# Kernel tuning notes

Hardware: AMD Instinct MI355X
Metric: run time of the kernel (lower is better)

The kernel has to match this reference:

```python
import jax, jax.numpy as jnp
import numpy as np

N, E, IN, HID, HEADS, OUT = 50000, 800000, 128, 32, 4, 2
NEG = 0.2   # LeakyReLU negative slope (PyG default)
EPS = 1e-5  # BatchNorm eps


def setup_inputs() -> dict:
    key = jax.random.key(0)
    ks = jax.random.split(key, 32)
    g = lambda i, shape, s=0.05: (jax.random.normal(ks[i], shape, jnp.float32) * s)
    d = {
        'x': jax.random.normal(ks[0], (N, IN), jnp.float32),
        'edge_index': jax.random.randint(ks[1], (2, E), 0, N, jnp.int32),
        'edge_attr': jax.random.normal(ks[2], (E, 1), jnp.float32),
        # conv1: GATv2, in=IN, out=HID, heads=HEADS, edge_dim=1
        'c1_Wl': g(3, (IN, HEADS * HID)), 'c1_bl': g(4, (HEADS * HID,)),
        'c1_Wr': g(5, (IN, HEADS * HID)), 'c1_br': g(6, (HEADS * HID,)),
        'c1_We': g(7, (1, HEADS * HID)),
        'c1_att': g(8, (HEADS, HID)),
        'c1_bias': g(9, (HEADS * HID,)),
        'bn1_gamma': jnp.ones((HEADS * HID,), jnp.float32),
        'bn1_beta': jnp.zeros((HEADS * HID,), jnp.float32),
        'bn1_mean': g(10, (HEADS * HID,)),
        'bn1_var': jax.random.uniform(ks[11], (HEADS * HID,), jnp.float32, 0.5, 1.5),
        # conv2: GATv2, in=HEADS*HID, out=HID, heads=1, edge_dim=1
        'c2_Wl': g(12, (HEADS * HID, HID)), 'c2_bl': g(13, (HID,)),
        'c2_Wr': g(14, (HEADS * HID, HID)), 'c2_br': g(15, (HID,)),
        'c2_We': g(16, (1, HID)),
        'c2_att': g(17, (1, HID)),
        'c2_bias': g(18, (HID,)),
        'bn2_gamma': jnp.ones((HID,), jnp.float32),
        'bn2_beta': jnp.zeros((HID,), jnp.float32),
        'bn2_mean': g(19, (HID,)),
        'bn2_var': jax.random.uniform(ks[20], (HID,), jnp.float32, 0.5, 1.5),
        # classifier
        'clf_W': g(21, (HID, OUT)), 'clf_b': g(22, (OUT,)),
    }
    return d


def _gatv2(x, src, dst, eattr, Wl, bl, Wr, br, We, att, bias, heads, out_ch, concat):
    n = x.shape[0]
    xl = (x @ Wl + bl).reshape(n, heads, out_ch)   # source transform
    xr = (x @ Wr + br).reshape(n, heads, out_ch)   # target transform
    el = (eattr @ We).reshape(-1, heads, out_ch)   # edge transform (no bias in PyG)
    s = xl[src] + xr[dst] + el                     # [E, H, C]
    s = jnp.where(s > 0, s, NEG * s)               # LeakyReLU
    logits = jnp.einsum('ehc,hc->eh', s, att)      # [E, H]
    # segment softmax over destination nodes (every node has a self-loop)
    m = jax.ops.segment_max(logits, dst, num_segments=n)
    a = jnp.exp(logits - m[dst])
    denom = jax.ops.segment_sum(a, dst, num_segments=n)
    alpha = a / denom[dst]                         # [E, H]
    out = jax.ops.segment_sum(alpha[:, :, None] * xl[src], dst, num_segments=n)
    out = out.reshape(n, heads * out_ch) if concat else out.mean(axis=1)
    return out + bias


def _bn_eval(x, gamma, beta, mean, var):
    return (x - mean) * (gamma / jnp.sqrt(var + EPS)) + beta


def reference(x, edge_index, edge_attr,
              c1_Wl, c1_bl, c1_Wr, c1_br, c1_We, c1_att, c1_bias,
              bn1_gamma, bn1_beta, bn1_mean, bn1_var,
              c2_Wl, c2_bl, c2_Wr, c2_br, c2_We, c2_att, c2_bias,
              bn2_gamma, bn2_beta, bn2_mean, bn2_var,
              clf_W, clf_b):
    n = x.shape[0]
    # add self-loops once (PyG GATv2 default add_self_loops=True, fill_value='mean')
    loop = jnp.arange(n, dtype=edge_index.dtype)
    src = jnp.concatenate([edge_index[0], loop])
    dst = jnp.concatenate([edge_index[1], loop])
    loop_attr = jnp.broadcast_to(edge_attr.mean(axis=0, keepdims=True), (n, edge_attr.shape[1]))
    eattr = jnp.concatenate([edge_attr, loop_attr], axis=0)

    h = _gatv2(x, src, dst, eattr, c1_Wl, c1_bl, c1_Wr, c1_br, c1_We, c1_att, c1_bias,
               HEADS, HID, True)
    h = jax.nn.relu(_bn_eval(h, bn1_gamma, bn1_beta, bn1_mean, bn1_var))
    # dropout inactive in eval mode
    h = _gatv2(h, src, dst, eattr, c2_Wl, c2_bl, c2_Wr, c2_br, c2_We, c2_att, c2_bias,
               1, HID, True)
    h = jax.nn.relu(_bn_eval(h, bn2_gamma, bn2_beta, bn2_mean, bn2_var))
    return h @ clf_W + clf_b
```

## Files before the change

### kernel.cpp

```cpp
#include <hip/hip_runtime.h>

#define NNODES 50000
#define NEDGES 800000
#define ETOT   850000
#define IN_CH  128
#define HID    32
#define HEADS  4
#define C1     128
#define NEG    0.2f
#define BNEPS  1e-5f
#define XFB2   1563
#define EHB    3125
#define WTS    160
#define XSS    136
#define NC     16
#define SCB    196

typedef __attribute__((ext_vector_type(8))) short short8;
typedef __attribute__((ext_vector_type(4))) float f32x4;

__device__ __forceinline__ unsigned short bf16r(float f) {
    unsigned u = __float_as_uint(f);
    return (unsigned short)((u + 0x7fffu + ((u >> 16) & 1u)) >> 16);
}
__device__ __forceinline__ unsigned bf16pair(float f0, float f1) {
    return (unsigned)bf16r(f0) | ((unsigned)bf16r(f1) << 16);
}
__device__ __forceinline__ float blo(unsigned u) { return __uint_as_float(u << 16); }
__device__ __forceinline__ float bhi(unsigned u) { return __uint_as_float(u & 0xffff0000u); }

__device__ __forceinline__ int block_iscan(int v, int* ls) {
    int lane = threadIdx.x & 63, w = threadIdx.x >> 6;
    #pragma unroll
    for (int o = 1; o < 64; o <<= 1) {
        int t = __shfl_up(v, o);
        if (lane >= o) v += t;
    }
    if (lane == 63) ls[w] = v;
    __syncthreads();
    int add = 0;
    #pragma unroll
    for (int i = 0; i < 4; i++) add += (i < w) ? ls[i] : 0;
    return v + add;
}

__global__ __launch_bounds__(256) void k_prep(const float* __restrict__ Wl,
                                              const float* __restrict__ Wr,
                                              unsigned short* __restrict__ WT) {
    int idx = blockIdx.x * 256 + threadIdx.x;
    int mat = idx >> 14, rem = idx & 16383;
    int k = rem >> 7, n = rem & 127;
    float v = mat ? Wr[k * 128 + n] : Wl[k * 128 + n];
    WT[(size_t)(mat * 128 + n) * WTS + k] = bf16r(v);
}

__global__ __launch_bounds__(256) void k_xf_eh(
    const float* __restrict__ x,
    const float* __restrict__ bl, const float* __restrict__ br,
    const unsigned short* __restrict__ WT,
    unsigned* __restrict__ xlb, float* __restrict__ xr,
    const int* __restrict__ ei, const float* __restrict__ ea,
    int* __restrict__ hist, float* __restrict__ meanbuf) {
    __shared__ short xs_s[64 * XSS];
    if (blockIdx.x >= XFB2) {
        float* ls = (float*)xs_s;
        int eb = blockIdx.x - XFB2;
        int e = eb * 256 + threadIdx.x;
        int c = eb & (NC - 1);
        float v = 0.f;
        if (e < NEDGES) {
            atomicAdd(&hist[c * NNODES + ei[NEDGES + e]], 1);
            v = ea[e];
        }
        #pragma unroll
        for (int o = 32; o > 0; o >>= 1) v += __shfl_down(v, o, 64);
        if ((threadIdx.x & 63) == 0) ls[threadIdx.x >> 6] = v;
        __syncthreads();
        if (threadIdx.x == 0) atomicAdd(meanbuf, ls[0] + ls[1] + ls[2] + ls[3]);
        return;
    }
    int n0g = blockIdx.x * 32;
    {
        int nd = threadIdx.x >> 3, kc = (threadIdx.x & 7) * 16;
        bool valid = (n0g + nd) < NNODES;
        float xv[16];
        #pragma unroll
        for (int i = 0; i < 4; i++) {
            float4 t = valid ? ((const float4*)(x + (size_t)(n0g + nd) * IN_CH + kc))[i]
                             : make_float4(0.f, 0.f, 0.f, 0.f);
            xv[4 * i] = t.x; xv[4 * i + 1] = t.y; xv[4 * i + 2] = t.z; xv[4 * i + 3] = t.w;
        }
        unsigned hi[8], lo[8];
        #pragma unroll
        for (int i = 0; i < 8; i++) {
            unsigned short h0 = bf16r(xv[2 * i]), h1 = bf16r(xv[2 * i + 1]);
            float l0 = xv[2 * i]     - __uint_as_float(((unsigned)h0) << 16);
            float l1 = xv[2 * i + 1] - __uint_as_float(((unsigned)h1) << 16);
            hi[i] = (unsigned)h0 | ((unsigned)h1 << 16);
            lo[i] = bf16pair(l0, l1);
        }
        uint4* ph = (uint4*)&xs_s[nd * XSS + kc];
        ph[0] = make_uint4(hi[0], hi[1], hi[2], hi[3]);
        ph[1] = make_uint4(hi[4], hi[5], hi[6], hi[7]);
        uint4* pl = (uint4*)&xs_s[(nd + 32) * XSS + kc];
        pl[0] = make_uint4(lo[0], lo[1], lo[2], lo[3]);
        pl[1] = make_uint4(lo[4], lo[5], lo[6], lo[7]);
    }
    __syncthreads();
    int lane = threadIdx.x & 63;
    int lm = lane & 15, q = lane >> 4;
    int w = threadIdx.x >> 6;
    int n0 = w * 64;
    f32x4 acc[2][4];
    #pragma unroll
    for (int mt = 0; mt < 2; mt++)
        #pragma unroll
        for (int nt = 0; nt < 4; nt++) acc[mt][nt] = (f32x4)0.f;

    #pragma unroll
    for (int ks = 0; ks < 4; ks++) {
        int k0 = ks * 32 + q * 8;
        short8 ah0 = *(const short8*)&xs_s[(lm)      * XSS + k0];
        short8 ah1 = *(const short8*)&xs_s[(16 + lm) * XSS + k0];
        short8 al0 = *(const short8*)&xs_s[(32 + lm) * XSS + k0];
        short8 al1 = *(const short8*)&xs_s[(48 + lm) * XSS + k0];
        #pragma unroll
        for (int nt = 0; nt < 4; nt++) {
            short8 bfr = *(const short8*)(WT + (size_t)(n0 + nt * 16 + lm) * WTS + k0);
            acc[0][nt] = __builtin_amdgcn_mfma_f32_16x16x32_bf16(al0, bfr, acc[0][nt], 0, 0, 0);
            acc[0][nt] = __builtin_amdgcn_mfma_f32_16x16x32_bf16(ah0, bfr, acc[0][nt], 0, 0, 0);
            acc[1][nt] = __builtin_amdgcn_mfma_f32_16x16x32_bf16(al1, bfr, acc[1][nt], 0, 0, 0);
            acc[1][nt] = __builtin_amdgcn_mfma_f32_16x16x32_bf16(ah1, bfr, acc[1][nt], 0, 0, 0);
        }
    }
    if (w < 2) {
        #pragma unroll
        for (int nt = 0; nt < 4; nt++) {
            int ch = n0 + nt * 16 + lm;
            float bv = bl[ch];
            #pragma unroll
            for (int mt = 0; mt < 2; mt++)
                #pragma unroll
                for (int r = 0; r < 4; r++) {
                    int node = n0g + mt * 16 + q * 4 + r;
                    float val = acc[mt][nt][r] + bv;
                    float pv = __shfl_xor(val, 1);
                    if ((lm & 1) == 0 && node < NNODES)
                        xlb[(size_t)node * 64 + (ch >> 1)] = bf16pair(val, pv);
                }
        }
    } else {
        #pragma unroll
        for (int nt = 0; nt < 4; nt++) {
            int ch = n0 - 128 + nt * 16 + lm;
            float bv = br[ch];
            #pragma unroll
            for (int mt = 0; mt < 2; mt++)
                #pragma unroll
                for (int r = 0; r < 4; r++) {
                    int node = n0g + mt * 16 + q * 4 + r;
                    if (node < NNODES)
                        xr[(size_t)node * C1 + ch] = acc[mt][nt][r] + bv;
                }
        }
    }
}

__global__ __launch_bounds__(256) void k_red(int* __restrict__ hist,
                                             int* __restrict__ deg,
                                             int* __restrict__ bsum) {
    __shared__ int ls[4];
    int d = blockIdx.x * 256 + threadIdx.x;
    int s = 0;
    if (d < NNODES) {
        #pragma unroll
        for (int c = 0; c < NC; c++) {
            int v = hist[c * NNODES + d];
            hist[c * NNODES + d] = s;
            s += v;
        }
        deg[d] = s;
    }
    int v = (d < NNODES) ? s + 1 : 0;
    #pragma unroll
    for (int o = 32; o > 0; o >>= 1) v += __shfl_down(v, o, 64);
    if ((threadIdx.x & 63) == 0) ls[threadIdx.x >> 6] = v;
    __syncthreads();
    if (threadIdx.x == 0) bsum[blockIdx.x] = ls[0] + ls[1] + ls[2] + ls[3];
}

__global__ __launch_bounds__(256) void k_bscan(const int* __restrict__ bsum,
                                               int* __restrict__ boff) {
    __shared__ int ls[4];
    int t = threadIdx.x;
    int v = (t < SCB) ? bsum[t] : 0;
    int incl = block_iscan(v, ls);
    if (t < SCB) boff[t] = incl - v;
}

__global__ __launch_bounds__(256) void k_rowp(const int* __restrict__ deg,
                                              const int* __restrict__ boff,
                                              int* __restrict__ rowptr) {
    __shared__ int ls[4];
    int d = blockIdx.x * 256 + threadIdx.x;
    int v = (d < NNODES) ? deg[d] + 1 : 0;
    int incl = block_iscan(v, ls);
    int base = boff[blockIdx.x];
    if (d < NNODES) rowptr[d] = base + incl - v;
    if (d == NNODES - 1) rowptr[NNODES] = base + incl;
}

__global__ __launch_bounds__(256) void k_fill(const int* __restrict__ ei,
                                              const float* __restrict__ ea,
                                              const int* __restrict__ rowptr,
                                              const float* __restrict__ meanbuf,
                                              int* __restrict__ hist,
                                              int2* __restrict__ cpack) {
    int e = blockIdx.x * 256 + threadIdx.x;
    if (e < NEDGES) {
        int d = ei[NEDGES + e];
        int c = (e >> 8) & (NC - 1);
        int off = atomicAdd(&hist[c * NNODES + d], 1);
        cpack[rowptr[d] + 1 + off] = make_int2(ei[e], __float_as_int(ea[e]));
    } else if (e < NEDGES + NNODES) {
        int i = e - NEDGES;
        cpack[rowptr[i]] = make_int2(i, __float_as_int(meanbuf[0] * (1.0f / NEDGES)));
    } else if (e < NEDGES + NNODES + 64) {
        cpack[ETOT + e - NEDGES - NNODES] = make_int2(0, 0);
    }
}

__global__ __launch_bounds__(256) void k_edge1(
    const unsigned* __restrict__ xlb, const float* __restrict__ xr,
    const int* __restrict__ rowptr, const int2* __restrict__ cpack,
    const float* __restrict__ We, const float* __restrict__ att,
    float* __restrict__ out1) {
    int node = blockIdx.x * 4 + (threadIdx.x >> 6);
    if (node >= NNODES) return;
    int lane = threadIdx.x & 63;
    int q = lane & 31, h = lane >> 5;
    int r0 = rowptr[node], r1 = rowptr[node + 1];
    float4 xrv = ((const float4*)xr)[(size_t)node * 32 + q];
    float4 wev = ((const float4*)We)[q];
    float4 atv = ((const float4*)att)[q];
    const uint2* xlv = (const uint2*)xlb;

    float den = 0.f, a0 = 0.f, a1 = 0.f, a2 = 0.f, a3 = 0.f;
    int nit = (r1 - r0 + 1) >> 1;
    int k = r0 + h;
    int2 sc = cpack[k];
    uint2 xv = xlv[(size_t)sc.x * 32 + q];
    for (int it = 0; it < nit; it++) {
        int2 scn = cpack[k + 2];
        uint2 xvn = xlv[(size_t)scn.x * 32 + q];
        bool ok = k < r1;
        float a = __int_as_float(sc.y);
        float x0 = blo(xv.x), x1 = bhi(xv.x), x2 = blo(xv.y), x3 = bhi(xv.y);
        float v0 = x0 + xrv.x + a * wev.x;  v0 = v0 > 0.f ? v0 : NEG * v0;
        float v1 = x1 + xrv.y + a * wev.y;  v1 = v1 > 0.f ? v1 : NEG * v1;
        float v2 = x2 + xrv.z + a * wev.z;  v2 = v2 > 0.f ? v2 : NEG * v2;
        float v3 = x3 + xrv.w + a * wev.w;  v3 = v3 > 0.f ? v3 : NEG * v3;
        float t = v0 * atv.x + v1 * atv.y + v2 * atv.z + v3 * atv.w;
        #pragma unroll
        for (int o = 4; o > 0; o >>= 1) t += __shfl_xor(t, o);
        float e = ok ? __expf(t) : 0.f;
        den += e;
        a0 = fmaf(e, x0, a0); a1 = fmaf(e, x1, a1);
        a2 = fmaf(e, x2, a2); a3 = fmaf(e, x3, a3);
        k += 2; sc = scn; xv = xvn;
    }
    den += __shfl_xor(den, 32);
    a0 += __shfl_xor(a0, 32); a1 += __shfl_xor(a1, 32);
    a2 += __shfl_xor(a2, 32); a3 += __shfl_xor(a3, 32);
    if (h == 0) {
        float rd = 1.f / den;
        ((float4*)out1)[(size_t)node * 32 + q] =
            make_float4(a0 * rd, a1 * rd, a2 * rd, a3 * rd);
    }
}

__global__ __launch_bounds__(256) void k_epi1(
    const float* __restrict__ out1, const float* __restrict__ bias1,
    const float* __restrict__ g1, const float* __restrict__ b1,
    const float* __restrict__ m1, const float* __restrict__ v1,
    const float* __restrict__ Wl2, const float* __restrict__ bl2,
    const float* __restrict__ Wr2, const float* __restrict__ br2,
    unsigned* __restrict__ xlb2, float* __restrict__ xr2) {
    __shared__ float hs[8 * 128];
    __shared__ float A[128], B[128];
    __shared__ float xs2[8 * 32];
    int n0 = blockIdx.x * 8;
    if (threadIdx.x < 128) {
        int c = threadIdx.x;
        float sc = g1[c] * rsqrtf(v1[c] + BNEPS);
        A[c] = sc;
        B[c] = (bias1[c] - m1[c]) * sc + b1[c];
    }
    __syncthreads();
    {
        float4 v = ((const float4*)(out1 + (size_t)n0 * C1))[threadIdx.x];
        int cb = (threadIdx.x * 4) & 127;
        float4 h;
        h.x = fmaxf(v.x * A[cb]     + B[cb],     0.f);
        h.y = fmaxf(v.y * A[cb + 1] + B[cb + 1], 0.f);
        h.z = fmaxf(v.z * A[cb + 2] + B[cb + 2], 0.f);
        h.w = fmaxf(v.w * A[cb + 3] + B[cb + 3], 0.f);
        ((float4*)hs)[threadIdx.x] = h;
    }
    __syncthreads();
    for (int o = threadIdx.x; o < 512; o += 256) {
        int node = o >> 6, rem = o & 63, mat = rem >> 5, c = rem & 31;
        const float* W = mat ? Wr2 : Wl2;
        float acc = mat ? br2[c] : bl2[c];
        const float4* hh = (const float4*)(hs + node * 128);
        #pragma unroll 8
        for (int k4 = 0; k4 < 32; k4++) {
            float4 hv = hh[k4];
            int kb = k4 * 4;
            acc += hv.x * W[kb * 32 + c]       + hv.y * W[(kb + 1) * 32 + c]
                 + hv.z * W[(kb + 2) * 32 + c] + hv.w * W[(kb + 3) * 32 + c];
        }
        if (mat) xr2[(size_t)(n0 + node) * HID + c] = acc;
        else     xs2[node * 32 + c] = acc;
    }
    __syncthreads();
    if (threadIdx.x < 128) {
        int nd = threadIdx.x >> 4, cc = threadIdx.x & 15;
        xlb2[(size_t)(n0 + nd) * 16 + cc] =
            bf16pair(xs2[nd * 32 + 2 * cc], xs2[nd * 32 + 2 * cc + 1]);
    }
}

__global__ __launch_bounds__(256) void k_edge2(
    const unsigned* __restrict__ xlb2, const float* __restrict__ xr2,
    const int* __restrict__ rowptr, const int2* __restrict__ cpack,
    const float* __restrict__ We2, const float* __restrict__ att2,
    const float* __restrict__ bias2,
    const float* __restrict__ g2, const float* __restrict__ b2,
    const float* __restrict__ m2, const float* __restrict__ v2,
    const float* __restrict__ W, const float* __restrict__ b,
    float* __restrict__ y) {
    int node = blockIdx.x * 4 + (threadIdx.x >> 6);
    if (node >= NNODES) return;
    int lane = threadIdx.x & 63;
    int q = lane & 7, s = lane >> 3;
    int r0 = rowptr[node], r1 = rowptr[node + 1];
    float4 xrv = ((const float4*)xr2)[(size_t)node * 8 + q];
    float4 wev = ((const float4*)We2)[q];
    float4 atv = ((const float4*)att2)[q];
    const uint2* xlv = (const uint2*)xlb2;

    float den = 0.f, a0 = 0.f, a1 = 0.f, a2 = 0.f, a3 = 0.f;
    int nit = (r1 - r0 + 7) >> 3;
    int k = r0 + s;
    int2 sc = cpack[k];
    uint2 xv = xlv[(size_t)sc.x * 8 + q];
    for (int it = 0; it < nit; it++) {
        int2 scn = cpack[k + 8];
        uint2 xvn = xlv[(size_t)scn.x * 8 + q];
        bool ok = k < r1;
        float a = __int_as_float(sc.y);
        float x0 = blo(xv.x), x1 = bhi(xv.x), x2 = blo(xv.y), x3 = bhi(xv.y);
        float v0 = x0 + xrv.x + a * wev.x;  v0 = v0 > 0.f ? v0 : NEG * v0;
        float v1 = x1 + xrv.y + a * wev.y;  v1 = v1 > 0.f ? v1 : NEG * v1;
        float v2 = x2 + xrv.z + a * wev.z;  v2 = v2 > 0.f ? v2 : NEG * v2;
        float v3 = x3 + xrv.w + a * wev.w;  v3 = v3 > 0.f ? v3 : NEG * v3;
        float t = v0 * atv.x + v1 * atv.y + v2 * atv.z + v3 * atv.w;
        #pragma unroll
        for (int o = 4; o > 0; o >>= 1) t += __shfl_xor(t, o);
        float e = ok ? __expf(t) : 0.f;
        den += e;
        a0 = fmaf(e, x0, a0); a1 = fmaf(e, x1, a1);
        a2 = fmaf(e, x2, a2); a3 = fmaf(e, x3, a3);
        k += 8; sc = scn; xv = xvn;
    }
    #pragma unroll
    for (int o = 8; o <= 32; o <<= 1) {
        den += __shfl_xor(den, o);
        a0 += __shfl_xor(a0, o); a1 += __shfl_xor(a1, o);
        a2 += __shfl_xor(a2, o); a3 += __shfl_xor(a3, o);
    }
    float rd = 1.f / den;
    float4 gv = ((const float4*)g2)[q],  bv = ((const float4*)b2)[q];
    float4 mv = ((const float4*)m2)[q],  vv = ((const float4*)v2)[q];
    float4 biv = ((const float4*)bias2)[q];
    float h0 = (a0 * rd + biv.x - mv.x) * (gv.x * rsqrtf(vv.x + BNEPS)) + bv.x;
    float h1 = (a1 * rd + biv.y - mv.y) * (gv.y * rsqrtf(vv.y + BNEPS)) + bv.y;
    float h2 = (a2 * rd + biv.z - mv.z) * (gv.z * rsqrtf(vv.z + BNEPS)) + bv.z;
    float h3 = (a3 * rd + biv.w - mv.w) * (gv.w * rsqrtf(vv.w + BNEPS)) + bv.w;
    h0 = fmaxf(h0, 0.f); h1 = fmaxf(h1, 0.f); h2 = fmaxf(h2, 0.f); h3 = fmaxf(h3, 0.f);
    float4 wa = ((const float4*)W)[2 * q];
    float4 wb = ((const float4*)W)[2 * q + 1];
    float t0 = h0 * wa.x + h1 * wa.z + h2 * wb.x + h3 * wb.z;
    float t1 = h0 * wa.y + h1 * wa.w + h2 * wb.y + h3 * wb.w;
    #pragma unroll
    for (int o = 4; o > 0; o >>= 1) {
        t0 += __shfl_xor(t0, o);
        t1 += __shfl_xor(t1, o);
    }
    if (lane == 0) {
        y[(size_t)node * 2]     = t0 + b[0];
        y[(size_t)node * 2 + 1] = t1 + b[1];
    }
}

extern "C" void kernel_launch(void* const* d_in, const int* in_sizes, int n_in,
                              void* d_out, int out_size, void* d_ws, size_t ws_size,
                              hipStream_t stream) {
    const float* x       = (const float*)d_in[0];
    const int*   ei      = (const int*)d_in[1];
    const float* ea      = (const float*)d_in[2];
    const float* c1_Wl   = (const float*)d_in[3];
    const float* c1_bl   = (const float*)d_in[4];
    const float* c1_Wr   = (const float*)d_in[5];
    const float* c1_br   = (const float*)d_in[6];
    const float* c1_We   = (const float*)d_in[7];
    const float* c1_att  = (const float*)d_in[8];
    const float* c1_bias = (const float*)d_in[9];
    const float* bn1_g   = (const float*)d_in[10];
    const float* bn1_b   = (const float*)d_in[11];
    const float* bn1_m   = (const float*)d_in[12];
    const float* bn1_v   = (const float*)d_in[13];
    const float* c2_Wl   = (const float*)d_in[14];
    const float* c2_bl   = (const float*)d_in[15];
    const float* c2_Wr   = (const float*)d_in[16];
    const float* c2_br   = (const float*)d_in[17];
    const float* c2_We   = (const float*)d_in[18];
    const float* c2_att  = (const float*)d_in[19];
    const float* c2_bias = (const float*)d_in[20];
    const float* bn2_g   = (const float*)d_in[21];
    const float* bn2_b   = (const float*)d_in[22];
    const float* bn2_m   = (const float*)d_in[23];
    const float* bn2_v   = (const float*)d_in[24];
    const float* clf_W   = (const float*)d_in[25];
    const float* clf_b   = (const float*)d_in[26];

    float* ws = (float*)d_ws;
    size_t off = 0;
    unsigned* XLb  = (unsigned*)(ws + off); off += (size_t)NNODES * 64;
    float*    XR1  = ws + off; off += (size_t)NNODES * C1;
    float*    OUT1 = ws + off; off += (size_t)NNODES * C1;
    unsigned* XLb2 = (unsigned*)(ws + off); off += (size_t)NNODES * 16;
    float*    XR2  = ws + off; off += (size_t)NNODES * HID;
    int2*     CPACK= (int2*)(ws + off); off += (size_t)(ETOT + 64) * 2;
    unsigned short* WT = (unsigned short*)(ws + off); off += 256 * WTS / 2;
    int*      ROWP = (int*)(ws + off); off += NNODES + 16;
    int*      DEG  = (int*)(ws + off); off += NNODES;
    int*      BSUM = (int*)(ws + off); off += 256;
    int*      BOFF = (int*)(ws + off); off += 256;
    int*      HIST = (int*)(ws + off); off += (size_t)NC * NNODES;
    float*    MEANB= ws + off; off += 64;
    if (ws_size < off * sizeof(float)) return;

    hipMemsetAsync(HIST, 0, ((size_t)NC * NNODES + 64) * sizeof(int), stream);
    k_prep  <<<128, 256, 0, stream>>>(c1_Wl, c1_Wr, WT);
    k_xf_eh <<<XFB2 + EHB, 256, 0, stream>>>(x, c1_bl, c1_br, WT, XLb, XR1,
                                             ei, ea, HIST, MEANB);
    k_red   <<<SCB, 256, 0, stream>>>(HIST, DEG, BSUM);
    k_bscan <<<1, 256, 0, stream>>>(BSUM, BOFF);
    k_rowp  <<<SCB, 256, 0, stream>>>(DEG, BOFF, ROWP);
    k_fill  <<<(NEDGES + NNODES + 64 + 255) / 256, 256, 0, stream>>>(ei, ea, ROWP, MEANB, HIST, CPACK);
    k_edge1 <<<(NNODES + 3) / 4, 256, 0, stream>>>(XLb, XR1, ROWP, CPACK, c1_We, c1_att, OUT1);
    k_epi1  <<<NNODES / 8, 256, 0, stream>>>(OUT1, c1_bias, bn1_g, bn1_b, bn1_m, bn1_v,
                                             c2_Wl, c2_bl, c2_Wr, c2_br, XLb2, XR2);
    k_edge2 <<<(NNODES + 3) / 4, 256, 0, stream>>>(XLb2, XR2, ROWP, CPACK, c2_We, c2_att,
                                                   c2_bias, bn2_g, bn2_b, bn2_m, bn2_v,
                                                   clf_W, clf_b, (float*)d_out);
}
```

Measured before the change: 359.6 us.

## Pack CSR entries into 32 bits and widen edge-kernel gathers to 16B

Each CSR entry shrinks from an int2 to a single 32-bit word: a 16-bit source index plus the edge attribute rounded to bf16. Both edge kernels now have each lane load 16B (8 channels) of the source features. This halves the lanes per node row, so twice as many edges are processed concurrently per wave, which is meant to cut gather traffic and raise memory-level parallelism. The fused transform/histogram kernel is also split back into two separate launches. The trade-offs are a lower-precision edge attribute, a hard limit of 65536 nodes from the 16-bit index, and one extra launch.

```diff
diff --git a/kernel.cpp b/kernel.cpp
--- a/kernel.cpp
+++ b/kernel.cpp
@@ -54,31 +54,31 @@
     WT[(size_t)(mat * 128 + n) * WTS + k] = bf16r(v);
 }
 
-__global__ __launch_bounds__(256) void k_xf_eh(
+__global__ __launch_bounds__(256) void k_eh(const int* __restrict__ ei,
+                                            const float* __restrict__ ea,
+                                            int* __restrict__ hist,
+                                            float* __restrict__ meanbuf) {
+    __shared__ float ls[4];
+    int e = blockIdx.x * 256 + threadIdx.x;
+    int c = blockIdx.x & (NC - 1);
+    float v = 0.f;
+    if (e < NEDGES) {
+        atomicAdd(&hist[c * NNODES + ei[NEDGES + e]], 1);
+        v = ea[e];
+    }
+    #pragma unroll
+    for (int o = 32; o > 0; o >>= 1) v += __shfl_down(v, o, 64);
+    if ((threadIdx.x & 63) == 0) ls[threadIdx.x >> 6] = v;
+    __syncthreads();
+    if (threadIdx.x == 0) atomicAdd(meanbuf, ls[0] + ls[1] + ls[2] + ls[3]);
+}
+
+__global__ __launch_bounds__(256) void k_xf(
     const float* __restrict__ x,
     const float* __restrict__ bl, const float* __restrict__ br,
     const unsigned short* __restrict__ WT,
-    unsigned* __restrict__ xlb, float* __restrict__ xr,
-    const int* __restrict__ ei, const float* __restrict__ ea,
-    int* __restrict__ hist, float* __restrict__ meanbuf) {
+    unsigned* __restrict__ xlb, float* __restrict__ xr) {
     __shared__ short xs_s[64 * XSS];
-    if (blockIdx.x >= XFB2) {
-        float* ls = (float*)xs_s;
-        int eb = blockIdx.x - XFB2;
-        int e = eb * 256 + threadIdx.x;
-        int c = eb & (NC - 1);
-        float v = 0.f;
-        if (e < NEDGES) {
-            atomicAdd(&hist[c * NNODES + ei[NEDGES + e]], 1);
-            v = ea[e];
-        }
-        #pragma unroll
-        for (int o = 32; o > 0; o >>= 1) v += __shfl_down(v, o, 64);
-        if ((threadIdx.x & 63) == 0) ls[threadIdx.x >> 6] = v;
-        __syncthreads();
-        if (threadIdx.x == 0) atomicAdd(meanbuf, ls[0] + ls[1] + ls[2] + ls[3]);
-        return;
-    }
     int n0g = blockIdx.x * 32;
     {
         int nd = threadIdx.x >> 3, kc = (threadIdx.x & 7) * 16;
@@ -215,67 +215,85 @@
                                               const int* __restrict__ rowptr,
                                               const float* __restrict__ meanbuf,
                                               int* __restrict__ hist,
-                                              int2* __restrict__ cpack) {
+                                              unsigned* __restrict__ cpack) {
     int e = blockIdx.x * 256 + threadIdx.x;
     if (e < NEDGES) {
         int d = ei[NEDGES + e];
         int c = (e >> 8) & (NC - 1);
         int off = atomicAdd(&hist[c * NNODES + d], 1);
-        cpack[rowptr[d] + 1 + off] = make_int2(ei[e], __float_as_int(ea[e]));
+        cpack[rowptr[d] + 1 + off] = ((unsigned)bf16r(ea[e]) << 16) | (unsigned)ei[e];
     } else if (e < NEDGES + NNODES) {
         int i = e - NEDGES;
-        cpack[rowptr[i]] = make_int2(i, __float_as_int(meanbuf[0] * (1.0f / NEDGES)));
+        cpack[rowptr[i]] = ((unsigned)bf16r(meanbuf[0] * (1.0f / NEDGES)) << 16) | (unsigned)i;
     } else if (e < NEDGES + NNODES + 64) {
-        cpack[ETOT + e - NEDGES - NNODES] = make_int2(0, 0);
+        cpack[ETOT + e - NEDGES - NNODES] = 0u;
     }
 }
 
 __global__ __launch_bounds__(256) void k_edge1(
     const unsigned* __restrict__ xlb, const float* __restrict__ xr,
-    const int* __restrict__ rowptr, const int2* __restrict__ cpack,
+    const int* __restrict__ rowptr, const unsigned* __restrict__ cpack,
     const float* __restrict__ We, const float* __restrict__ att,
     float* __restrict__ out1) {
     int node = blockIdx.x * 4 + (threadIdx.x >> 6);
     if (node >= NNODES) return;
     int lane = threadIdx.x & 63;
-    int q = lane & 31, h = lane >> 5;
+    int q = lane & 15, s = lane >> 4;
     int r0 = rowptr[node], r1 = rowptr[node + 1];
-    float4 xrv = ((const float4*)xr)[(size_t)node * 32 + q];
-    float4 wev = ((const float4*)We)[q];
-    float4 atv = ((const float4*)att)[q];
-    const uint2* xlv = (const uint2*)xlb;
-
-    float den = 0.f, a0 = 0.f, a1 = 0.f, a2 = 0.f, a3 = 0.f;
-    int nit = (r1 - r0 + 1) >> 1;
-    int k = r0 + h;
-    int2 sc = cpack[k];
-    uint2 xv = xlv[(size_t)sc.x * 32 + q];
+    float4 xr0 = ((const float4*)xr)[(size_t)node * 32 + 2 * q];
+    float4 xr1 = ((const float4*)xr)[(size_t)node * 32 + 2 * q + 1];
+    float4 we0 = ((const float4*)We)[2 * q],  we1 = ((const float4*)We)[2 * q + 1];
+    float4 at0 = ((const float4*)att)[2 * q], at1 = ((const float4*)att)[2 * q + 1];
+    const uint4* xlv = (const uint4*)xlb;
+
+    float den = 0.f;
+    float a0 = 0.f, a1 = 0.f, a2 = 0.f, a3 = 0.f;
+    float a4 = 0.f, a5 = 0.f, a6 = 0.f, a7 = 0.f;
+    int nit = (r1 - r0 + 3) >> 2;
+    int k = r0 + s;
+    unsigned sc = cpack[k];
+    uint4 xv = xlv[(size_t)(sc & 0xffffu) * 16 + q];
     for (int it = 0; it < nit; it++) {
-        int2 scn = cpack[k + 2];
-        uint2 xvn = xlv[(size_t)scn.x * 32 + q];
+        unsigned scn = cpack[k + 4];
+        uint4 xvn = xlv[(size_t)(scn & 0xffffu) * 16 + q];
         bool ok = k < r1;
-        float a = __int_as_float(sc.y);
+        float av = __uint_as_float(sc & 0xffff0000u);
         float x0 = blo(xv.x), x1 = bhi(xv.x), x2 = blo(xv.y), x3 = bhi(xv.y);
-        float v0 = x0 + xrv.x + a * wev.x;  v0 = v0 > 0.f ? v0 : NEG * v0;
-        float v1 = x1 + xrv.y + a * wev.y;  v1 = v1 > 0.f ? v1 : NEG * v1;
-        float v2 = x2 + xrv.z + a * wev.z;  v2 = v2 > 0.f ? v2 : NEG * v2;
-        float v3 = x3 + xrv.w + a * wev.w;  v3 = v3 > 0.f ? v3 : NEG * v3;
-        float t = v0 * atv.x + v1 * atv.y + v2 * atv.z + v3 * atv.w;
-        #pragma unroll
-        for (int o = 4; o > 0; o >>= 1) t += __shfl_xor(t, o);
+        float x4 = blo(xv.z), x5 = bhi(xv.z), x6 = blo(xv.w), x7 = bhi(xv.w);
+        float v0 = x0 + xr0.x + av * we0.x;  v0 = v0 > 0.f ? v0 : NEG * v0;
+        float v1 = x1 + xr0.y + av * we0.y;  v1 = v1 > 0.f ? v1 : NEG * v1;
+        float v2 = x2 + xr0.z + av * we0.z;  v2 = v2 > 0.f ? v2 : NEG * v2;
+        float v3 = x3 + xr0.w + av * we0.w;  v3 = v3 > 0.f ? v3 : NEG * v3;
+        float v4 = x4 + xr1.x + av * we1.x;  v4 = v4 > 0.f ? v4 : NEG * v4;
+        float v5 = x5 + xr1.y + av * we1.y;  v5 = v5 > 0.f ? v5 : NEG * v5;
+        float v6 = x6 + xr1.z + av * we1.z;  v6 = v6 > 0.f ? v6 : NEG * v6;
+        float v7 = x7 + xr1.w + av * we1.w;  v7 = v7 > 0.f ? v7 : NEG * v7;
+        float t = v0 * at0.x + v1 * at0.y + v2 * at0.z + v3 * at0.w
+                + v4 * at1.x + v5 * at1.y + v6 * at1.z + v7 * at1.w;
+        t += __shfl_xor(t, 1);
+        t += __shfl_xor(t, 2);
         float e = ok ? __expf(t) : 0.f;
         den += e;
         a0 = fmaf(e, x0, a0); a1 = fmaf(e, x1, a1);
         a2 = fmaf(e, x2, a2); a3 = fmaf(e, x3, a3);
-        k += 2; sc = scn; xv = xvn;
-    }
-    den += __shfl_xor(den, 32);
-    a0 += __shfl_xor(a0, 32); a1 += __shfl_xor(a1, 32);
-    a2 += __shfl_xor(a2, 32); a3 += __shfl_xor(a3, 32);
-    if (h == 0) {
+        a4 = fmaf(e, x4, a4); a5 = fmaf(e, x5, a5);
+        a6 = fmaf(e, x6, a6); a7 = fmaf(e, x7, a7);
+        k += 4; sc = scn; xv = xvn;
+    }
+    #pragma unroll
+    for (int o = 16; o <= 32; o <<= 1) {
+        den += __shfl_xor(den, o);
+        a0 += __shfl_xor(a0, o); a1 += __shfl_xor(a1, o);
+        a2 += __shfl_xor(a2, o); a3 += __shfl_xor(a3, o);
+        a4 += __shfl_xor(a4, o); a5 += __shfl_xor(a5, o);
+        a6 += __shfl_xor(a6, o); a7 += __shfl_xor(a7, o);
+    }
+    if (s == 0) {
         float rd = 1.f / den;
-        ((float4*)out1)[(size_t)node * 32 + q] =
+        ((float4*)out1)[(size_t)node * 32 + 2 * q] =
             make_float4(a0 * rd, a1 * rd, a2 * rd, a3 * rd);
+        ((float4*)out1)[(size_t)node * 32 + 2 * q + 1] =
+            make_float4(a4 * rd, a5 * rd, a6 * rd, a7 * rd);
     }
 }
 
@@ -333,7 +351,7 @@
 
 __global__ __launch_bounds__(256) void k_edge2(
     const unsigned* __restrict__ xlb2, const float* __restrict__ xr2,
-    const int* __restrict__ rowptr, const int2* __restrict__ cpack,
+    const int* __restrict__ rowptr, const unsigned* __restrict__ cpack,
     const float* __restrict__ We2, const float* __restrict__ att2,
     const float* __restrict__ bias2,
     const float* __restrict__ g2, const float* __restrict__ b2,
@@ -343,61 +361,82 @@
     int node = blockIdx.x * 4 + (threadIdx.x >> 6);
     if (node >= NNODES) return;
     int lane = threadIdx.x & 63;
-    int q = lane & 7, s = lane >> 3;
+    int q = lane & 3, s = lane >> 2;
     int r0 = rowptr[node], r1 = rowptr[node + 1];
-    float4 xrv = ((const float4*)xr2)[(size_t)node * 8 + q];
-    float4 wev = ((const float4*)We2)[q];
-    float4 atv = ((const float4*)att2)[q];
-    const uint2* xlv = (const uint2*)xlb2;
-
-    float den = 0.f, a0 = 0.f, a1 = 0.f, a2 = 0.f, a3 = 0.f;
-    int nit = (r1 - r0 + 7) >> 3;
+    float4 xr0 = ((const float4*)xr2)[(size_t)node * 8 + 2 * q];
+    float4 xr1 = ((const float4*)xr2)[(size_t)node * 8 + 2 * q + 1];
+    float4 we0 = ((const float4*)We2)[2 * q],  we1 = ((const float4*)We2)[2 * q + 1];
+    float4 at0 = ((const float4*)att2)[2 * q], at1 = ((const float4*)att2)[2 * q + 1];
+    const uint4* xlv = (const uint4*)xlb2;
+
+    float den = 0.f;
+    float a0 = 0.f, a1 = 0.f, a2 = 0.f, a3 = 0.f;
+    float a4 = 0.f, a5 = 0.f, a6 = 0.f, a7 = 0.f;
+    int nit = (r1 - r0 + 15) >> 4;
     int k = r0 + s;
-    int2 sc = cpack[k];
-    uint2 xv = xlv[(size_t)sc.x * 8 + q];
+    unsigned sc = cpack[k];
+    uint4 xv = xlv[(size_t)(sc & 0xffffu) * 4 + q];
     for (int it = 0; it < nit; it++) {
-        int2 scn = cpack[k + 8];
-        uint2 xvn = xlv[(size_t)scn.x * 8 + q];
+        unsigned scn = cpack[k + 16];
+        uint4 xvn = xlv[(size_t)(scn & 0xffffu) * 4 + q];
         bool ok = k < r1;
-        float a = __int_as_float(sc.y);
+        float av = __uint_as_float(sc & 0xffff0000u);
         float x0 = blo(xv.x), x1 = bhi(xv.x), x2 = blo(xv.y), x3 = bhi(xv.y);
-        float v0 = x0 + xrv.x + a * wev.x;  v0 = v0 > 0.f ? v0 : NEG * v0;
-        float v1 = x1 + xrv.y + a * wev.y;  v1 = v1 > 0.f ? v1 : NEG * v1;
-        float v2 = x2 + xrv.z + a * wev.z;  v2 = v2 > 0.f ? v2 : NEG * v2;
-        float v3 = x3 + xrv.w + a * wev.w;  v3 = v3 > 0.f ? v3 : NEG * v3;
-        float t = v0 * atv.x + v1 * atv.y + v2 * atv.z + v3 * atv.w;
-        #pragma unroll
-        for (int o = 4; o > 0; o >>= 1) t += __shfl_xor(t, o);
+        float x4 = blo(xv.z), x5 = bhi(xv.z), x6 = blo(xv.w), x7 = bhi(xv.w);
+        float v0 = x0 + xr0.x + av * we0.x;  v0 = v0 > 0.f ? v0 : NEG * v0;
+        float v1 = x1 + xr0.y + av * we0.y;  v1 = v1 > 0.f ? v1 : NEG * v1;
+        float v2 = x2 + xr0.z + av * we0.z;  v2 = v2 > 0.f ? v2 : NEG * v2;
+        float v3 = x3 + xr0.w + av * we0.w;  v3 = v3 > 0.f ? v3 : NEG * v3;
+        float v4 = x4 + xr1.x + av * we1.x;  v4 = v4 > 0.f ? v4 : NEG * v4;
+        float v5 = x5 + xr1.y + av * we1.y;  v5 = v5 > 0.f ? v5 : NEG * v5;
+        float v6 = x6 + xr1.z + av * we1.z;  v6 = v6 > 0.f ? v6 : NEG * v6;
+        float v7 = x7 + xr1.w + av * we1.w;  v7 = v7 > 0.f ? v7 : NEG * v7;
+        float t = v0 * at0.x + v1 * at0.y + v2 * at0.z + v3 * at0.w
+                + v4 * at1.x + v5 * at1.y + v6 * at1.z + v7 * at1.w;
+        t += __shfl_xor(t, 1);
+        t += __shfl_xor(t, 2);
         float e = ok ? __expf(t) : 0.f;
         den += e;
         a0 = fmaf(e, x0, a0); a1 = fmaf(e, x1, a1);
         a2 = fmaf(e, x2, a2); a3 = fmaf(e, x3, a3);
-        k += 8; sc = scn; xv = xvn;
-    }
-    #pragma unroll
-    for (int o = 8; o <= 32; o <<= 1) {
+        a4 = fmaf(e, x4, a4); a5 = fmaf(e, x5, a5);
+        a6 = fmaf(e, x6, a6); a7 = fmaf(e, x7, a7);
+        k += 16; sc = scn; xv = xvn;
+    }
+    #pragma unroll
+    for (int o = 4; o <= 32; o <<= 1) {
         den += __shfl_xor(den, o);
         a0 += __shfl_xor(a0, o); a1 += __shfl_xor(a1, o);
         a2 += __shfl_xor(a2, o); a3 += __shfl_xor(a3, o);
+        a4 += __shfl_xor(a4, o); a5 += __shfl_xor(a5, o);
+        a6 += __shfl_xor(a6, o); a7 += __shfl_xor(a7, o);
     }
     float rd = 1.f / den;
-    float4 gv = ((const float4*)g2)[q],  bv = ((const float4*)b2)[q];
-    float4 mv = ((const float4*)m2)[q],  vv = ((const float4*)v2)[q];
-    float4 biv = ((const float4*)bias2)[q];
-    float h0 = (a0 * rd + biv.x - mv.x) * (gv.x * rsqrtf(vv.x + BNEPS)) + bv.x;
-    float h1 = (a1 * rd + biv.y - mv.y) * (gv.y * rsqrtf(vv.y + BNEPS)) + bv.y;
-    float h2 = (a2 * rd + biv.z - mv.z) * (gv.z * rsqrtf(vv.z + BNEPS)) + bv.z;
-    float h3 = (a3 * rd + biv.w - mv.w) * (gv.w * rsqrtf(vv.w + BNEPS)) + bv.w;
+    float4 gv0 = ((const float4*)g2)[2 * q],    gv1 = ((const float4*)g2)[2 * q + 1];
+    float4 bv0 = ((const float4*)b2)[2 * q],    bv1 = ((const float4*)b2)[2 * q + 1];
+    float4 mv0 = ((const float4*)m2)[2 * q],    mv1 = ((const float4*)m2)[2 * q + 1];
+    float4 vv0 = ((const float4*)v2)[2 * q],    vv1 = ((const float4*)v2)[2 * q + 1];
+    float4 bi0 = ((const float4*)bias2)[2 * q], bi1 = ((const float4*)bias2)[2 * q + 1];
+    float h0 = (a0 * rd + bi0.x - mv0.x) * (gv0.x * rsqrtf(vv0.x + BNEPS)) + bv0.x;
+    float h1 = (a1 * rd + bi0.y - mv0.y) * (gv0.y * rsqrtf(vv0.y + BNEPS)) + bv0.y;
+    float h2 = (a2 * rd + bi0.z - mv0.z) * (gv0.z * rsqrtf(vv0.z + BNEPS)) + bv0.z;
+    float h3 = (a3 * rd + bi0.w - mv0.w) * (gv0.w * rsqrtf(vv0.w + BNEPS)) + bv0.w;
+    float h4 = (a4 * rd + bi1.x - mv1.x) * (gv1.x * rsqrtf(vv1.x + BNEPS)) + bv1.x;
+    float h5 = (a5 * rd + bi1.y - mv1.y) * (gv1.y * rsqrtf(vv1.y + BNEPS)) + bv1.y;
+    float h6 = (a6 * rd + bi1.z - mv1.z) * (gv1.z * rsqrtf(vv1.z + BNEPS)) + bv1.z;
+    float h7 = (a7 * rd + bi1.w - mv1.w) * (gv1.w * rsqrtf(vv1.w + BNEPS)) + bv1.w;
     h0 = fmaxf(h0, 0.f); h1 = fmaxf(h1, 0.f); h2 = fmaxf(h2, 0.f); h3 = fmaxf(h3, 0.f);
-    float4 wa = ((const float4*)W)[2 * q];
-    float4 wb = ((const float4*)W)[2 * q + 1];
-    float t0 = h0 * wa.x + h1 * wa.z + h2 * wb.x + h3 * wb.z;
-    float t1 = h0 * wa.y + h1 * wa.w + h2 * wb.y + h3 * wb.w;
-    #pragma unroll
-    for (int o = 4; o > 0; o >>= 1) {
-        t0 += __shfl_xor(t0, o);
-        t1 += __shfl_xor(t1, o);
-    }
+    h4 = fmaxf(h4, 0.f); h5 = fmaxf(h5, 0.f); h6 = fmaxf(h6, 0.f); h7 = fmaxf(h7, 0.f);
+    float4 w0 = ((const float4*)W)[4 * q];
+    float4 w1 = ((const float4*)W)[4 * q + 1];
+    float4 w2 = ((const float4*)W)[4 * q + 2];
+    float4 w3 = ((const float4*)W)[4 * q + 3];
+    float t0 = h0 * w0.x + h1 * w0.z + h2 * w1.x + h3 * w1.z
+             + h4 * w2.x + h5 * w2.z + h6 * w3.x + h7 * w3.z;
+    float t1 = h0 * w0.y + h1 * w0.w + h2 * w1.y + h3 * w1.w
+             + h4 * w2.y + h5 * w2.w + h6 * w3.y + h7 * w3.w;
+    t0 += __shfl_xor(t0, 1); t0 += __shfl_xor(t0, 2);
+    t1 += __shfl_xor(t1, 1); t1 += __shfl_xor(t1, 2);
     if (lane == 0) {
         y[(size_t)node * 2]     = t0 + b[0];
         y[(size_t)node * 2 + 1] = t1 + b[1];
@@ -442,7 +481,7 @@
     float*    OUT1 = ws + off; off += (size_t)NNODES * C1;
     unsigned* XLb2 = (unsigned*)(ws + off); off += (size_t)NNODES * 16;
     float*    XR2  = ws + off; off += (size_t)NNODES * HID;
-    int2*     CPACK= (int2*)(ws + off); off += (size_t)(ETOT + 64) * 2;
+    unsigned* CPACK= (unsigned*)(ws + off); off += (size_t)ETOT + 64;
     unsigned short* WT = (unsigned short*)(ws + off); off += 256 * WTS / 2;
     int*      ROWP = (int*)(ws + off); off += NNODES + 16;
     int*      DEG  = (int*)(ws + off); off += NNODES;
@@ -454,8 +493,8 @@
 
     hipMemsetAsync(HIST, 0, ((size_t)NC * NNODES + 64) * sizeof(int), stream);
     k_prep  <<<128, 256, 0, stream>>>(c1_Wl, c1_Wr, WT);
-    k_xf_eh <<<XFB2 + EHB, 256, 0, stream>>>(x, c1_bl, c1_br, WT, XLb, XR1,
-                                             ei, ea, HIST, MEANB);
+    k_eh    <<<EHB, 256, 0, stream>>>(ei, ea, HIST, MEANB);
+    k_xf    <<<XFB2, 256, 0, stream>>>(x, c1_bl, c1_br, WT, XLb, XR1);
     k_red   <<<SCB, 256, 0, stream>>>(HIST, DEG, BSUM);
     k_bscan <<<1, 256, 0, stream>>>(BSUM, BOFF);
     k_rowp  <<<SCB, 256, 0, stream>>>(DEG, BOFF, ROWP);
```

Result: slower. 388.0 us (+7.9%).
